# Performance work log

Hardware: AMD Instinct MI355X
Metric: run time of the kernel (lower is better)

Reference implementation:

```python
import jax, jax.numpy as jnp
import numpy as np

T, B, E, H = 2048, 2, 1024, 16
DH = E // H
SCALE = DH ** -0.5
NEG = jnp.finfo(jnp.float32).min


def setup_inputs() -> dict:
    key = jax.random.key(0)
    ks = jax.random.split(key, 10)
    s = 0.02
    query = jax.random.normal(ks[0], (T, B, E), dtype=jnp.float32)
    key_padding_mask = jax.random.randint(ks[1], (B, T), 0, 2).astype(bool)
    # causal additive mask, broadcastable over (bsz, heads, tgt, src)
    causal = jnp.triu(jnp.ones((T, T), dtype=bool), k=1)
    attn_mask = jnp.where(causal, NEG, 0.0).astype(jnp.float32)[None, None]
    Wq = jax.random.normal(ks[2], (E, E), jnp.float32) * s
    bq = jax.random.normal(ks[3], (E,), jnp.float32) * s
    Wk = jax.random.normal(ks[4], (E, E), jnp.float32) * s
    bk = jax.random.normal(ks[5], (E,), jnp.float32) * s
    Wv = jax.random.normal(ks[6], (E, E), jnp.float32) * s
    bv = jax.random.normal(ks[7], (E,), jnp.float32) * s
    Wo = jax.random.normal(ks[8], (E, E), jnp.float32) * s
    bo = jax.random.normal(ks[9], (E,), jnp.float32) * s
    return {"query": query, "key_padding_mask": key_padding_mask, "attn_mask": attn_mask,
            "Wq": Wq, "bq": bq, "Wk": Wk, "bk": bk, "Wv": Wv, "bv": bv, "Wo": Wo, "bo": bo}


def _heads(x):
    # [T, B, E] -> [B, H, T, DH]
    return x.reshape(T, B, H, DH).transpose(1, 2, 0, 3)


def reference(query, key_padding_mask, attn_mask, Wq, bq, Wk, bk, Wv, bv, Wo, bo):
    # projections (torch Linear: x @ W.T + b); q scaled as in module
    q = _heads((query @ Wq.T + bq) * SCALE)          # [B,H,T,DH]
    k = _heads(query @ Wk.T + bk)                    # [B,H,S,DH] (self-attn: S=T)
    v = _heads(query @ Wv.T + bv)
    scores = jnp.einsum('bhtd,bhsd->bhts', q, k)     # [B,H,T,S]
    scores = scores + attn_mask                      # additive causal mask
    # key_padding_mask True -> masked_fill with dtype min
    scores = jnp.where(key_padding_mask[:, None, None, :], NEG, scores)
    probs = jax.nn.softmax(scores, axis=-1)
    ctx = jnp.einsum('bhts,bhsd->bhtd', probs, v)    # [B,H,T,DH]
    ctx = ctx.transpose(2, 0, 1, 3).reshape(T, B, E) # back to [T,B,E]
    return ctx @ Wo.T + bo
```

## Files before the change

kernel.cpp:

```cpp
#include <hip/hip_runtime.h>
#include <hip/hip_bf16.h>
#include <stdint.h>

typedef unsigned short u16;
typedef uint32_t u32;
typedef unsigned long long u64;
typedef __attribute__((ext_vector_type(8))) short bf16x8;
typedef __attribute__((ext_vector_type(4))) float f32x4;
typedef __attribute__((ext_vector_type(16))) float f32x16;
typedef __attribute__((ext_vector_type(4))) u32 u32x4;

#define T_SEQ 2048

__device__ __forceinline__ float bf2f(u16 u) {
  union { u32 i; float f; } v; v.i = ((u32)u) << 16; return v.f;
}
__device__ __forceinline__ u16 f2bf(float f) {
  union { float f; u32 i; } v; v.f = f;
  u32 u = v.i;
  return (u16)((u + 0x7fffu + ((u >> 16) & 1u)) >> 16);
}

#if __has_builtin(__builtin_amdgcn_exp2f)
#define EXP2F(x) __builtin_amdgcn_exp2f(x)
#else
#define EXP2F(x) exp2f(x)
#endif

__device__ __forceinline__ u32 permpack(float lo, float hi) {
#if __has_builtin(__builtin_amdgcn_perm)
  return __builtin_amdgcn_perm(__float_as_uint(hi), __float_as_uint(lo), 0x07060302u);
#else
  return (__float_as_uint(hi) & 0xFFFF0000u) | (__float_as_uint(lo) >> 16);
#endif
}

__device__ __forceinline__ void gload_lds16(const void* g, void* l) {
  __builtin_amdgcn_global_load_lds(
      (const __attribute__((address_space(1))) void*)g,
      (__attribute__((address_space(3))) void*)l, 16, 0, 0);
}

__global__ __launch_bounds__(256) void cvt_kernel(const float* __restrict__ src,
                                                  u16* __restrict__ dst, int n) {
  int i = (blockIdx.x * 256 + threadIdx.x) * 4;
  if (i + 3 < n) {
    const float4 v = *(const float4*)(src + i);
    ushort4 o;
    o.x = f2bf(v.x); o.y = f2bf(v.y); o.z = f2bf(v.z); o.w = f2bf(v.w);
    *(ushort4*)(dst + i) = o;
  }
}

__global__ __launch_bounds__(256) void cvt4_kernel(
    const float* __restrict__ s0, const float* __restrict__ s1,
    const float* __restrict__ s2, const float* __restrict__ s3,
    u16* __restrict__ dst) {
  const int z = blockIdx.y;
  const float* src = (z == 0) ? s0 : (z == 1) ? s1 : (z == 2) ? s2 : s3;
  int i = (blockIdx.x * 256 + threadIdx.x) * 4;
  const float4 v = *(const float4*)(src + i);
  ushort4 o;
  o.x = f2bf(v.x); o.y = f2bf(v.y); o.z = f2bf(v.z); o.w = f2bf(v.w);
  *(ushort4*)(dst + (size_t)z * 1048576 + i) = o;
}

__device__ __forceinline__ void gemm_core_128x128(
    f32x4 acc[2][4], const u16* __restrict__ A, const u16* __restrict__ Bw,
    int bm, int bn, u16* As, u16* Bs)
{
  const int tid = threadIdx.x;
  const int w = tid >> 6, lane = tid & 63, g = lane >> 4, c = lane & 15;
  const int wr = (w & 3) * 32, wc = (w >> 2) * 64;
  for (int k0 = 0; k0 < 1024; k0 += 64) {
    __syncthreads();
    #pragma unroll
    for (int is = 0; is < 2; ++is) {
      int o = (is*8 + w)*1024 + lane*16;
      int row = o >> 7, c16 = (o >> 4) & 7;
      gload_lds16(A + (size_t)(bm*128 + row)*1024 + k0 + (c16 ^ (row & 7))*8,
                  (char*)As + (is*8 + w)*1024);
    }
    #pragma unroll
    for (int is = 0; is < 2; ++is) {
      int o = (is*8 + w)*1024 + lane*16;
      int row = o >> 7, c16 = (o >> 4) & 7;
      gload_lds16(Bw + (size_t)(bn*128 + row)*1024 + k0 + (c16 ^ (row & 7))*8,
                  (char*)Bs + (is*8 + w)*1024);
    }
    __syncthreads();
    bf16x8 af[2][2], bfr[4][2];
    #pragma unroll
    for (int mf = 0; mf < 2; ++mf)
      #pragma unroll
      for (int kc = 0; kc < 2; ++kc) {
        int row = wr + mf*16 + c;
        int colb = kc*64 + g*16;
        af[mf][kc] = *(const bf16x8*)((const char*)As + row*128 + (colb ^ ((row & 7) << 4)));
      }
    #pragma unroll
    for (int nf = 0; nf < 4; ++nf)
      #pragma unroll
      for (int kc = 0; kc < 2; ++kc) {
        int row = wc + nf*16 + c;
        int colb = kc*64 + g*16;
        bfr[nf][kc] = *(const bf16x8*)((const char*)Bs + row*128 + (colb ^ ((row & 7) << 4)));
      }
    #pragma unroll
    for (int mf = 0; mf < 2; ++mf)
      #pragma unroll
      for (int nf = 0; nf < 4; ++nf)
        #pragma unroll
        for (int kc = 0; kc < 2; ++kc)
          acc[mf][nf] = __builtin_amdgcn_mfma_f32_16x16x32_bf16(
              af[mf][kc], bfr[nf][kc], acc[mf][nf], 0, 0, 0);
  }
}

__global__ __launch_bounds__(512, 2) void gemm_qkv(
    const u16* __restrict__ Abf, const u16* __restrict__ Wbf,
    const float* __restrict__ bq, const float* __restrict__ bk,
    const float* __restrict__ bv, u16* __restrict__ qkvh)
{
  __shared__ __align__(16) u16 As[128*64];
  __shared__ __align__(16) u16 Bs[128*64];
  f32x4 acc[2][4];
  #pragma unroll
  for (int mf = 0; mf < 2; ++mf)
    #pragma unroll
    for (int nf = 0; nf < 4; ++nf) acc[mf][nf] = (f32x4){0.f,0.f,0.f,0.f};
  const int bx = blockIdx.x;
  const int bm = (bx & 7) * 4 + (bx >> 3);
  gemm_core_128x128(acc, Abf, Wbf, bm, blockIdx.y, As, Bs);
  const int tid = threadIdx.x, w = tid >> 6, lane = tid & 63, g = lane >> 4, c = lane & 15;
  const int wr = (w & 3) * 32, wc = (w >> 2) * 64;
  #pragma unroll
  for (int mf = 0; mf < 2; ++mf)
    #pragma unroll
    for (int nf = 0; nf < 4; ++nf) {
      int col = blockIdx.y*128 + wc + nf*16 + c;
      int z = col >> 10, colz = col & 1023;
      const float* bias = (z == 0) ? bq : (z == 1) ? bk : bv;
      float bcol = bias[colz];
      float scl = (z == 0) ? 0.18033688011112043f : 1.0f;
      int h = colz >> 6, d = colz & 63;
      u16* dst = qkvh + (size_t)z * 4194304;
      #pragma unroll
      for (int r = 0; r < 4; ++r) {
        int row = bm*128 + wr + mf*16 + g*4 + r;
        int t = row >> 1, bb = row & 1;
        float v = (acc[mf][nf][r] + bcol) * scl;
        dst[(size_t)(bb*16 + h)*131072 + (size_t)t*64 + d] = f2bf(v);
      }
    }
}

__global__ __launch_bounds__(512, 2) void gemm_out(
    const u16* __restrict__ ctx2, const u16* __restrict__ Wobf,
    const float* __restrict__ bo, float* __restrict__ out)
{
  __shared__ __align__(16) u16 As[128*64];
  __shared__ __align__(16) u16 Bs[128*64];
  f32x4 acc[2][4];
  #pragma unroll
  for (int mf = 0; mf < 2; ++mf)
    #pragma unroll
    for (int nf = 0; nf < 4; ++nf) acc[mf][nf] = (f32x4){0.f,0.f,0.f,0.f};
  const int bx = blockIdx.x;
  const int bm = (bx & 7) * 4 + (bx >> 3);
  gemm_core_128x128(acc, ctx2, Wobf, bm, blockIdx.y, As, Bs);
  const int tid = threadIdx.x, w = tid >> 6, lane = tid & 63, g = lane >> 4, c = lane & 15;
  const int wr = (w & 3) * 32, wc = (w >> 2) * 64;
  #pragma unroll
  for (int mf = 0; mf < 2; ++mf)
    #pragma unroll
    for (int nf = 0; nf < 4; ++nf) {
      int col = blockIdx.y*128 + wc + nf*16 + c;
      float bcol = bo[col];
      #pragma unroll
      for (int r = 0; r < 4; ++r) {
        int row = bm*128 + wr + mf*16 + g*4 + r;
        out[(size_t)row*1024 + col] = acc[mf][nf][r] + bcol;
      }
    }
}

__global__ __launch_bounds__(256) void vtrans_kernel(const u16* __restrict__ Vh,
                                                     u16* __restrict__ Vt,
                                                     float* __restrict__ vs) {
  __shared__ u16 tile[64][72];
  const int bh = blockIdx.x >> 5, tc = blockIdx.x & 31;
  const int t0 = tc * 64;
  const int tid = threadIdx.x;
  {
    const int tl = tid >> 2, d0 = (tid & 3) * 16;
    const u16* src = Vh + (size_t)bh*131072 + (size_t)(t0 + tl)*64 + d0;
    bf16x8 a = *(const bf16x8*)src;
    bf16x8 b2 = *(const bf16x8*)(src + 8);
    #pragma unroll
    for (int j = 0; j < 8; ++j) {
      tile[d0 + j][tl] = (u16)a[j];
      tile[d0 + 8 + j][tl] = (u16)b2[j];
    }
  }
  __syncthreads();
  {
    const int d = tid >> 2, tq = (tid & 3) * 16;
    bf16x8 o0, o1;
    float s = 0.f;
    #pragma unroll
    for (int j = 0; j < 8; ++j) {
      u16 x0 = tile[d][tq + j], x1 = tile[d][tq + 8 + j];
      o0[j] = (short)x0; o1[j] = (short)x1;
      s += bf2f(x0) + bf2f(x1);
    }
    u16* dst = Vt + (size_t)bh*131072 + (size_t)d*2048 + t0 + tq;
    *(bf16x8*)dst = o0;
    *(bf16x8*)(dst + 8) = o1;
    s += __shfl_xor(s, 1, 64);
    s += __shfl_xor(s, 2, 64);
    if ((tid & 3) == 0) atomicAdd(&vs[bh*64 + d], s);
  }
}

#define ZERO16 (f32x16){0.f,0.f,0.f,0.f,0.f,0.f,0.f,0.f,0.f,0.f,0.f,0.f,0.f,0.f,0.f,0.f}
#define NEGINF (-__builtin_inff())

__global__ __launch_bounds__(256, 2) void flash_attn(
    const u16* __restrict__ Qh, const u16* __restrict__ Kh,
    const u16* __restrict__ Vt, const int* __restrict__ kpm,
    const float* __restrict__ vsum, u16* __restrict__ ctx2,
    u16* __restrict__ pctx, float* __restrict__ pml)
{
  __shared__ __align__(16) u16 Kl[2][4096];
  __shared__ __align__(16) u16 Vl[2][4096];

  const int tid = threadIdx.x;
  const int w = tid >> 6, lane = tid & 63;
  const int l31 = lane & 31, hi = lane >> 5;

  const int id = blockIdx.x;
  const int xcd = id & 7, rest = id >> 3;
  const int bh = xcd * 4 + (rest & 3);
  const int pr = rest >> 2;
  const u64 k0t = 0x9AA5BBCC6DDEE7FFULL, k1t = 0x94883210ULL;
  const u64 m0t = 0x0102101021010210ULL, m1t = 0x12102222ULL;
  const int k  = (int)(((pr < 16) ? (k0t >> (pr*4)) : (k1t >> ((pr-16)*4))) & 15);
  const int md = (int)(((pr < 16) ? (m0t >> (pr*4)) : (m1t >> ((pr-16)*4))) & 3);
  const int NS = (md == 2) ? 1 : 2, ch = md & 1;

  const int ntmax = 2*k + 2;
  const int b = bh >> 4, h = bh & 15;
  const size_t hbase = (size_t)bh * 131072;
  int lo, hicap;
  if (NS == 1) { lo = 0; hicap = ntmax; }
  else { lo = ch ? (k+1) : 0; hicap = ch ? ntmax : (k+1); }
  const int q = 128*k + 32*w + l31;
  const int myNt = 2*k + 1 + (w >> 1);

  bf16x8 qfrag[4];
  #pragma unroll
  for (int kt = 0; kt < 4; ++kt)
    qfrag[kt] = *(const bf16x8*)(Qh + hbase + (size_t)q*64 + kt*16 + hi*8);

  {
    const int s0t = lo * 64;
    const int jb = (w & 1) * 4;
    if (w < 2) {
      #pragma unroll
      for (int is = 0; is < 4; ++is) {
        int o = (jb + is)*1024 + lane*16;
        int row = o >> 7, c16 = (o >> 4) & 7;
        gload_lds16(Kh + hbase + (size_t)(s0t + row)*64 + (c16 ^ (row & 7))*8,
                    (char*)Kl[0] + (jb + is)*1024);
      }
    } else {
      #pragma unroll
      for (int is = 0; is < 4; ++is) {
        int o = (jb + is)*1024 + lane*16;
        int row = o >> 7, c16 = (o >> 4) & 7;
        gload_lds16(Vt + hbase + (size_t)row*2048 + s0t + (c16 ^ (row & 7))*8,
                    (char*)Vl[0] + (jb + is)*1024);
      }
    }
  }
  int kpmv_cur = kpm[b*T_SEQ + lo*64 + lane];
  int kpmv_nxt = 0;
  __syncthreads();

  float mrow = NEGINF, lrow = 0.f;
  f32x16 cacc0 = ZERO16, cacc1 = ZERO16;

  for (int t = lo; t < hicap; ++t) {
    const int cur = (t - lo) & 1, nxt = cur ^ 1;
    const int s0 = t * 64;
    const bool notLast = (t + 1 < hicap);
    const bool diag = (t >= myNt - 1);

    if (notLast) {
      const int s0n = s0 + 64;
      const int jb = (w & 1) * 4;
      if (w < 2) {
        #pragma unroll
        for (int is = 0; is < 4; ++is) {
          int o = (jb + is)*1024 + lane*16;
          int row = o >> 7, c16 = (o >> 4) & 7;
          gload_lds16(Kh + hbase + (size_t)(s0n + row)*64 + (c16 ^ (row & 7))*8,
                      (char*)Kl[nxt] + (jb + is)*1024);
        }
      } else {
        #pragma unroll
        for (int is = 0; is < 4; ++is) {
          int o = (jb + is)*1024 + lane*16;
          int row = o >> 7, c16 = (o >> 4) & 7;
          gload_lds16(Vt + hbase + (size_t)row*2048 + s0n + (c16 ^ (row & 7))*8,
                      (char*)Vl[nxt] + (jb + is)*1024);
        }
      }
      kpmv_nxt = kpm[b*T_SEQ + s0n + lane];
    }

    bf16x8 kreg[2][4], vf[2][4];
    #pragma unroll
    for (int sub = 0; sub < 2; ++sub)
      #pragma unroll
      for (int kt = 0; kt < 4; ++kt) {
        int row = sub*32 + l31;
        int colb = kt*32 + hi*16;
        kreg[sub][kt] = *(const bf16x8*)((const char*)Kl[cur] + row*128 + (colb ^ ((row & 7) << 4)));
        vf[sub][kt]   = *(const bf16x8*)((const char*)Vl[cur] + row*128 + (colb ^ ((row & 7) << 4)));
      }

    f32x16 st0 = ZERO16, st1 = ZERO16;
    __builtin_amdgcn_s_setprio(1);
    #pragma unroll
    for (int kt = 0; kt < 4; ++kt) {
      st0 = __builtin_amdgcn_mfma_f32_32x32x16_bf16(kreg[0][kt], qfrag[kt], st0, 0, 0, 0);
      st1 = __builtin_amdgcn_mfma_f32_32x32x16_bf16(kreg[1][kt], qfrag[kt], st1, 0, 0, 0);
    }
    __builtin_amdgcn_s_setprio(0);

    {
      const u64 mask = __ballot(kpmv_cur != 0);
      const u32 m0 = (u32)mask, m1 = (u32)(mask >> 32);
      const u64 m4 = mask >> 4;
      const u32 m4l = (u32)m4, m4h = (u32)(m4 >> 32);
      const u32 w0 = hi ? m4l : m0;
      const u32 w1 = hi ? m4h : m1;
      const int lim = q - s0 - 4*hi;
      #pragma unroll
      for (int m = 0; m < 4; ++m) {
        u32 nib0 = (w0 >> (m*8)) & 15u;
        u32 nib1 = (w1 >> (m*8)) & 15u;
        if (diag) {
          int t0c = lim - m*8;       int c0 = min(max(t0c + 1, 0), 4);
          int t1c = lim - 32 - m*8;  int c1 = min(max(t1c + 1, 0), 4);
          nib0 |= (0xFu << c0) & 0xFu;
          nib1 |= (0xFu << c1) & 0xFu;
        }
        #pragma unroll
        for (int r = 0; r < 4; ++r) {
          if ((nib0 >> r) & 1) st0[m*4 + r] = NEGINF;
          if ((nib1 >> r) & 1) st1[m*4 + r] = NEGINF;
        }
      }
      float t8[8];
      #pragma unroll
      for (int i = 0; i < 8; ++i)
        t8[i] = fmaxf(fmaxf(st0[i], st0[i+8]), fmaxf(st1[i], st1[i+8]));
      float t4a = fmaxf(t8[0], t8[4]), t4b = fmaxf(t8[1], t8[5]);
      float t4c = fmaxf(t8[2], t8[6]), t4d = fmaxf(t8[3], t8[7]);
      float rm = fmaxf(fmaxf(t4a, t4b), fmaxf(t4c, t4d));
      rm = fmaxf(rm, __shfl_xor(rm, 32, 64));

      const bool need = (rm > mrow + 8.f) || (mrow < -1e30f);
      if (__any(need)) {
        const float mn = fmaxf(mrow, rm);
        const float sc = (mn < -1e30f) ? 1.f : EXP2F(mrow - mn);
        mrow = mn;
        lrow *= sc;
        #pragma unroll
        for (int i = 0; i < 16; ++i) { cacc0[i] *= sc; cacc1[i] *= sc; }
      }
      const bool dead = (mrow < -1e30f);
      float a0 = 0.f, a1 = 0.f, a2 = 0.f, a3 = 0.f;
      #pragma unroll
      for (int i = 0; i < 16; i += 4) {
        float p0 = dead ? 0.f : EXP2F(st0[i+0] - mrow); st0[i+0] = p0; a0 += p0;
        float p1 = dead ? 0.f : EXP2F(st0[i+1] - mrow); st0[i+1] = p1; a1 += p1;
        float p2 = dead ? 0.f : EXP2F(st0[i+2] - mrow); st0[i+2] = p2; a2 += p2;
        float p3 = dead ? 0.f : EXP2F(st0[i+3] - mrow); st0[i+3] = p3; a3 += p3;
      }
      #pragma unroll
      for (int i = 0; i < 16; i += 4) {
        float p0 = dead ? 0.f : EXP2F(st1[i+0] - mrow); st1[i+0] = p0; a0 += p0;
        float p1 = dead ? 0.f : EXP2F(st1[i+1] - mrow); st1[i+1] = p1; a1 += p1;
        float p2 = dead ? 0.f : EXP2F(st1[i+2] - mrow); st1[i+2] = p2; a2 += p2;
        float p3 = dead ? 0.f : EXP2F(st1[i+3] - mrow); st1[i+3] = p3; a3 += p3;
      }
      float ps = (a0 + a1) + (a2 + a3);
      ps += __shfl_xor(ps, 32, 64);
      lrow += ps;
    }

    u32 pk[8][2];
    #pragma unroll
    for (int m = 0; m < 4; ++m) {
      pk[m][0]   = permpack(st0[m*4+0], st0[m*4+1]);
      pk[m][1]   = permpack(st0[m*4+2], st0[m*4+3]);
      pk[4+m][0] = permpack(st1[m*4+0], st1[m*4+1]);
      pk[4+m][1] = permpack(st1[m*4+2], st1[m*4+3]);
    }
    bf16x8 pf[4];
    #pragma unroll
    for (int ks = 0; ks < 4; ++ks) {
      u32 own0 = pk[2*ks][0],   own1 = pk[2*ks][1];
      u32 oth0 = pk[2*ks+1][0], oth1 = pk[2*ks+1][1];
      u32 r0 = __shfl_xor(hi ? own0 : oth0, 32, 64);
      u32 r1 = __shfl_xor(hi ? own1 : oth1, 32, 64);
      u32 w0 = hi ? r0 : own0;
      u32 w1 = hi ? r1 : own1;
      u32 w2 = hi ? oth0 : r0;
      u32 w3 = hi ? oth1 : r1;
      u32x4 wv = {w0, w1, w2, w3};
      pf[ks] = __builtin_bit_cast(bf16x8, wv);
    }

    __builtin_amdgcn_s_setprio(1);
    #pragma unroll
    for (int ks = 0; ks < 4; ++ks)
      cacc0 = __builtin_amdgcn_mfma_f32_32x32x16_bf16(vf[0][ks], pf[ks], cacc0, 0, 0, 0);
    #pragma unroll
    for (int ks = 0; ks < 4; ++ks)
      cacc1 = __builtin_amdgcn_mfma_f32_32x32x16_bf16(vf[1][ks], pf[ks], cacc1, 0, 0, 0);
    __builtin_amdgcn_s_setprio(0);

    kpmv_cur = kpmv_nxt;
    if (notLast) __syncthreads();
  }

  if (NS == 1) {
    const bool dead = (lrow == 0.f);
    const float rl = dead ? 0.f : 1.f / lrow;
    #pragma unroll
    for (int subd = 0; subd < 2; ++subd) {
      #pragma unroll
      for (int m = 0; m < 4; ++m) {
        const int d0 = subd*32 + hi*4 + m*8;
        float v0 = (subd ? cacc1[m*4+0] : cacc0[m*4+0]) * rl;
        float v1 = (subd ? cacc1[m*4+1] : cacc0[m*4+1]) * rl;
        float v2 = (subd ? cacc1[m*4+2] : cacc0[m*4+2]) * rl;
        float v3 = (subd ? cacc1[m*4+3] : cacc0[m*4+3]) * rl;
        if (dead) {
          const float* vs = vsum + bh*64 + d0;
          v0 = vs[0] * (1.0f/2048.0f);
          v1 = vs[1] * (1.0f/2048.0f);
          v2 = vs[2] * (1.0f/2048.0f);
          v3 = vs[3] * (1.0f/2048.0f);
        }
        ushort4 o;
        o.x = f2bf(v0); o.y = f2bf(v1); o.z = f2bf(v2); o.w = f2bf(v3);
        *(ushort4*)(ctx2 + (size_t)(q*2 + b)*1024 + h*64 + d0) = o;
      }
    }
  } else {
    const int slot = ((bh << 3) + (k - 8))*2 + ch;
    const int row = w*32 + l31;
    u16* pc = pctx + ((size_t)slot*128 + row)*64;
    #pragma unroll
    for (int subd = 0; subd < 2; ++subd) {
      #pragma unroll
      for (int m = 0; m < 4; ++m) {
        const int d0 = subd*32 + hi*4 + m*8;
        const f32x16& cc = subd ? cacc1 : cacc0;
        ushort4 o;
        o.x = f2bf(cc[m*4+0]); o.y = f2bf(cc[m*4+1]);
        o.z = f2bf(cc[m*4+2]); o.w = f2bf(cc[m*4+3]);
        *(ushort4*)(pc + d0) = o;
      }
    }
    if (!hi) {
      float2 ml; ml.x = mrow; ml.y = lrow;
      *(float2*)(pml + ((size_t)slot*128 + row)*2) = ml;
    }
  }
}

__global__ __launch_bounds__(64) void combine_kernel(
    const u16* __restrict__ pctx, const float* __restrict__ pml,
    const float* __restrict__ vsum, u16* __restrict__ ctx2)
{
  const int qtm = blockIdx.x, bh = blockIdx.y;
  const int qt = 32 + qtm;
  const int k = qt >> 2, wq = qt & 3;
  const int b = bh >> 4, h = bh & 15;
  const int lane = threadIdx.x;
  const int qr = lane >> 1, d0 = (lane & 1) * 32;
  const int slot0 = ((bh << 3) + (k - 8))*2;
  const int row = wq*32 + qr;
  const float* ml0 = pml + ((size_t)slot0*128 + row)*2;
  const float* ml1 = pml + ((size_t)(slot0+1)*128 + row)*2;
  const float m1 = ml0[0], l1 = ml0[1];
  const float m2 = ml1[0], l2 = ml1[1];
  const float ms = fmaxf(m1, m2);
  bool dead = (ms == NEGINF);
  const float w1 = dead ? 0.f : EXP2F(m1 - ms);
  const float w2 = dead ? 0.f : EXP2F(m2 - ms);
  const float lt = w1*l1 + w2*l2;
  dead = dead || (lt == 0.f);
  const float rl = dead ? 0.f : 1.f / lt;
  const u16* c1 = pctx + ((size_t)slot0*128 + row)*64 + d0;
  const u16* c2 = pctx + ((size_t)(slot0+1)*128 + row)*64 + d0;
  const int qrow = qt*32 + qr;
  u16* dst = ctx2 + (size_t)(qrow*2 + b)*1024 + h*64 + d0;
  #pragma unroll
  for (int g2 = 0; g2 < 4; ++g2) {
    bf16x8 a = *(const bf16x8*)(c1 + g2*8);
    bf16x8 bb = *(const bf16x8*)(c2 + g2*8);
    bf16x8 o;
    #pragma unroll
    for (int j = 0; j < 8; ++j) {
      float v = (w1*bf2f((u16)a[j]) + w2*bf2f((u16)bb[j])) * rl;
      if (dead) v = vsum[bh*64 + d0 + g2*8 + j] * (1.0f/2048.0f);
      o[j] = (short)f2bf(v);
    }
    *(bf16x8*)(dst + g2*8) = o;
  }
}

extern "C" void kernel_launch(void* const* d_in, const int* in_sizes, int n_in,
                              void* d_out, int out_size, void* d_ws, size_t ws_size,
                              hipStream_t stream) {
  const float* query = (const float*)d_in[0];
  const int*   kpm   = (const int*)d_in[1];
  const float* Wq = (const float*)d_in[3];
  const float* bq = (const float*)d_in[4];
  const float* Wk = (const float*)d_in[5];
  const float* bk = (const float*)d_in[6];
  const float* Wv = (const float*)d_in[7];
  const float* bv = (const float*)d_in[8];
  const float* Wo = (const float*)d_in[9];
  const float* bo = (const float*)d_in[10];

  char* ws = (char*)d_ws;
  u16*   qbf  = (u16*)(ws);
  u16*   Vt   = (u16*)(ws);
  u16*   wbf  = (u16*)(ws + 8388608);
  u16*   qkvh = (u16*)(ws + 16777216);
  u16*   pctx = (u16*)(ws + 33554432);
  u16*   ctx2 = (u16*)(ws + 41943040);
  float* vsum = (float*)(ws + 50331648);
  float* pml  = (float*)(ws + 50339840);

  cvt_kernel<<<dim3(4096), 256, 0, stream>>>(query, qbf, 4194304);
  cvt4_kernel<<<dim3(1024, 4), 256, 0, stream>>>(Wq, Wk, Wv, Wo, wbf);

  hipMemsetAsync(vsum, 0, 2048 * sizeof(float), stream);

  gemm_qkv<<<dim3(32, 24), 512, 0, stream>>>(qbf, wbf, bq, bk, bv, qkvh);
  vtrans_kernel<<<dim3(1024), 256, 0, stream>>>(qkvh + 2*4194304, Vt, vsum);
  flash_attn<<<dim3(768), 256, 0, stream>>>(qkvh, qkvh + 1*4194304,
                                            Vt, kpm, vsum, ctx2, pctx, pml);
  combine_kernel<<<dim3(32, 32), 64, 0, stream>>>(pctx, pml, vsum, ctx2);
  gemm_out<<<dim3(32, 8), 512, 0, stream>>>(ctx2, wbf + 3*1048576, bo, (float*)d_out);
}
```

Baseline: 134.4 us.

## Double-buffer GEMM LDS tiles, premask scores via accumulator init, use permlane32 swaps

```diff
diff --git a/kernel.cpp b/kernel.cpp
--- a/kernel.cpp
+++ b/kernel.cpp
@@ -8,6 +8,7 @@
 typedef __attribute__((ext_vector_type(8))) short bf16x8;
 typedef __attribute__((ext_vector_type(4))) float f32x4;
 typedef __attribute__((ext_vector_type(16))) float f32x16;
+typedef __attribute__((ext_vector_type(2))) unsigned int u32x2;
 typedef __attribute__((ext_vector_type(4))) u32 u32x4;
 
 #define T_SEQ 2048
@@ -33,6 +34,24 @@
 #else
   return (__float_as_uint(hi) & 0xFFFF0000u) | (__float_as_uint(lo) >> 16);
 #endif
+}
+
+__device__ __forceinline__ void plswap(u32& a, u32& b) {
+#if __has_builtin(__builtin_amdgcn_permlane32_swap)
+  u32x2 r = __builtin_amdgcn_permlane32_swap(a, b, false, false);
+  a = r[0]; b = r[1];
+#else
+  u32 ra = __shfl_xor(a, 32, 64), rb = __shfl_xor(b, 32, 64);
+  const bool hi_ = (threadIdx.x & 32) != 0;
+  u32 na = hi_ ? rb : a;
+  u32 nb = hi_ ? b : ra;
+  a = na; b = nb;
+#endif
+}
+__device__ __forceinline__ float othhalf(float x, bool ishi) {
+  u32 a = __float_as_uint(x), b = a;
+  plswap(a, b);
+  return __uint_as_float(ishi ? a : b);
 }
 
 __device__ __forceinline__ void gload_lds16(const void* g, void* l) {
@@ -72,23 +91,33 @@
   const int tid = threadIdx.x;
   const int w = tid >> 6, lane = tid & 63, g = lane >> 4, c = lane & 15;
   const int wr = (w & 3) * 32, wc = (w >> 2) * 64;
-  for (int k0 = 0; k0 < 1024; k0 += 64) {
-    __syncthreads();
+
+  auto stage = [&](int buf, int k0) {
     #pragma unroll
     for (int is = 0; is < 2; ++is) {
       int o = (is*8 + w)*1024 + lane*16;
       int row = o >> 7, c16 = (o >> 4) & 7;
       gload_lds16(A + (size_t)(bm*128 + row)*1024 + k0 + (c16 ^ (row & 7))*8,
-                  (char*)As + (is*8 + w)*1024);
+                  (char*)As + buf*16384 + (is*8 + w)*1024);
     }
     #pragma unroll
     for (int is = 0; is < 2; ++is) {
       int o = (is*8 + w)*1024 + lane*16;
       int row = o >> 7, c16 = (o >> 4) & 7;
       gload_lds16(Bw + (size_t)(bn*128 + row)*1024 + k0 + (c16 ^ (row & 7))*8,
-                  (char*)Bs + (is*8 + w)*1024);
-    }
-    __syncthreads();
+                  (char*)Bs + buf*16384 + (is*8 + w)*1024);
+    }
+  };
+
+  stage(0, 0);
+  asm volatile("s_waitcnt vmcnt(0)" ::: "memory");
+  __syncthreads();
+
+  for (int k0 = 0; k0 < 1024; k0 += 64) {
+    const int cur = (k0 >> 6) & 1, nxt = cur ^ 1;
+    const bool more = (k0 + 64 < 1024);
+    if (more) stage(nxt, k0 + 64);
+
     bf16x8 af[2][2], bfr[4][2];
     #pragma unroll
     for (int mf = 0; mf < 2; ++mf)
@@ -96,7 +125,7 @@
       for (int kc = 0; kc < 2; ++kc) {
         int row = wr + mf*16 + c;
         int colb = kc*64 + g*16;
-        af[mf][kc] = *(const bf16x8*)((const char*)As + row*128 + (colb ^ ((row & 7) << 4)));
+        af[mf][kc] = *(const bf16x8*)((const char*)As + cur*16384 + row*128 + (colb ^ ((row & 7) << 4)));
       }
     #pragma unroll
     for (int nf = 0; nf < 4; ++nf)
@@ -104,7 +133,7 @@
       for (int kc = 0; kc < 2; ++kc) {
         int row = wc + nf*16 + c;
         int colb = kc*64 + g*16;
-        bfr[nf][kc] = *(const bf16x8*)((const char*)Bs + row*128 + (colb ^ ((row & 7) << 4)));
+        bfr[nf][kc] = *(const bf16x8*)((const char*)Bs + cur*16384 + row*128 + (colb ^ ((row & 7) << 4)));
       }
     #pragma unroll
     for (int mf = 0; mf < 2; ++mf)
@@ -114,6 +143,11 @@
         for (int kc = 0; kc < 2; ++kc)
           acc[mf][nf] = __builtin_amdgcn_mfma_f32_16x16x32_bf16(
               af[mf][kc], bfr[nf][kc], acc[mf][nf], 0, 0, 0);
+
+    if (more) {
+      asm volatile("s_waitcnt vmcnt(0)" ::: "memory");
+      __syncthreads();
+    }
   }
 }
 
@@ -122,8 +156,8 @@
     const float* __restrict__ bq, const float* __restrict__ bk,
     const float* __restrict__ bv, u16* __restrict__ qkvh)
 {
-  __shared__ __align__(16) u16 As[128*64];
-  __shared__ __align__(16) u16 Bs[128*64];
+  __shared__ __align__(16) u16 As[2][128*64];
+  __shared__ __align__(16) u16 Bs[2][128*64];
   f32x4 acc[2][4];
   #pragma unroll
   for (int mf = 0; mf < 2; ++mf)
@@ -131,7 +165,7 @@
     for (int nf = 0; nf < 4; ++nf) acc[mf][nf] = (f32x4){0.f,0.f,0.f,0.f};
   const int bx = blockIdx.x;
   const int bm = (bx & 7) * 4 + (bx >> 3);
-  gemm_core_128x128(acc, Abf, Wbf, bm, blockIdx.y, As, Bs);
+  gemm_core_128x128(acc, Abf, Wbf, bm, blockIdx.y, &As[0][0], &Bs[0][0]);
   const int tid = threadIdx.x, w = tid >> 6, lane = tid & 63, g = lane >> 4, c = lane & 15;
   const int wr = (w & 3) * 32, wc = (w >> 2) * 64;
   #pragma unroll
@@ -159,8 +193,8 @@
     const u16* __restrict__ ctx2, const u16* __restrict__ Wobf,
     const float* __restrict__ bo, float* __restrict__ out)
 {
-  __shared__ __align__(16) u16 As[128*64];
-  __shared__ __align__(16) u16 Bs[128*64];
+  __shared__ __align__(16) u16 As[2][128*64];
+  __shared__ __align__(16) u16 Bs[2][128*64];
   f32x4 acc[2][4];
   #pragma unroll
   for (int mf = 0; mf < 2; ++mf)
@@ -168,7 +202,7 @@
     for (int nf = 0; nf < 4; ++nf) acc[mf][nf] = (f32x4){0.f,0.f,0.f,0.f};
   const int bx = blockIdx.x;
   const int bm = (bx & 7) * 4 + (bx >> 3);
-  gemm_core_128x128(acc, ctx2, Wobf, bm, blockIdx.y, As, Bs);
+  gemm_core_128x128(acc, ctx2, Wobf, bm, blockIdx.y, &As[0][0], &Bs[0][0]);
   const int tid = threadIdx.x, w = tid >> 6, lane = tid & 63, g = lane >> 4, c = lane & 15;
   const int wr = (w & 3) * 32, wc = (w >> 2) * 64;
   #pragma unroll
@@ -320,50 +354,56 @@
       kpmv_nxt = kpm[b*T_SEQ + s0n + lane];
     }
 
-    bf16x8 kreg[2][4], vf[2][4];
-    #pragma unroll
-    for (int sub = 0; sub < 2; ++sub)
-      #pragma unroll
-      for (int kt = 0; kt < 4; ++kt) {
-        int row = sub*32 + l31;
-        int colb = kt*32 + hi*16;
-        kreg[sub][kt] = *(const bf16x8*)((const char*)Kl[cur] + row*128 + (colb ^ ((row & 7) << 4)));
-        vf[sub][kt]   = *(const bf16x8*)((const char*)Vl[cur] + row*128 + (colb ^ ((row & 7) << 4)));
-      }
-
-    f32x16 st0 = ZERO16, st1 = ZERO16;
-    __builtin_amdgcn_s_setprio(1);
-    #pragma unroll
-    for (int kt = 0; kt < 4; ++kt) {
-      st0 = __builtin_amdgcn_mfma_f32_32x32x16_bf16(kreg[0][kt], qfrag[kt], st0, 0, 0, 0);
-      st1 = __builtin_amdgcn_mfma_f32_32x32x16_bf16(kreg[1][kt], qfrag[kt], st1, 0, 0, 0);
-    }
-    __builtin_amdgcn_s_setprio(0);
-
+    u32 kill0 = 0, kill1 = 0;
     {
       const u64 mask = __ballot(kpmv_cur != 0);
       const u32 m0 = (u32)mask, m1 = (u32)(mask >> 32);
       const u64 m4 = mask >> 4;
       const u32 m4l = (u32)m4, m4h = (u32)(m4 >> 32);
-      const u32 w0 = hi ? m4l : m0;
-      const u32 w1 = hi ? m4h : m1;
+      const u32 w0m = hi ? m4l : m0;
+      const u32 w1m = hi ? m4h : m1;
       const int lim = q - s0 - 4*hi;
       #pragma unroll
       for (int m = 0; m < 4; ++m) {
-        u32 nib0 = (w0 >> (m*8)) & 15u;
-        u32 nib1 = (w1 >> (m*8)) & 15u;
+        u32 nib0 = (w0m >> (m*8)) & 15u;
+        u32 nib1 = (w1m >> (m*8)) & 15u;
         if (diag) {
           int t0c = lim - m*8;       int c0 = min(max(t0c + 1, 0), 4);
           int t1c = lim - 32 - m*8;  int c1 = min(max(t1c + 1, 0), 4);
           nib0 |= (0xFu << c0) & 0xFu;
           nib1 |= (0xFu << c1) & 0xFu;
         }
-        #pragma unroll
-        for (int r = 0; r < 4; ++r) {
-          if ((nib0 >> r) & 1) st0[m*4 + r] = NEGINF;
-          if ((nib1 >> r) & 1) st1[m*4 + r] = NEGINF;
-        }
-      }
+        kill0 |= nib0 << (m*4);
+        kill1 |= nib1 << (m*4);
+      }
+    }
+    f32x16 st0, st1;
+    #pragma unroll
+    for (int i = 0; i < 16; ++i) {
+      st0[i] = ((kill0 >> i) & 1u) ? NEGINF : 0.f;
+      st1[i] = ((kill1 >> i) & 1u) ? NEGINF : 0.f;
+    }
+
+    bf16x8 kreg[2][4], vf[2][4];
+    #pragma unroll
+    for (int sub = 0; sub < 2; ++sub)
+      #pragma unroll
+      for (int kt = 0; kt < 4; ++kt) {
+        int row = sub*32 + l31;
+        int colb = kt*32 + hi*16;
+        kreg[sub][kt] = *(const bf16x8*)((const char*)Kl[cur] + row*128 + (colb ^ ((row & 7) << 4)));
+        vf[sub][kt]   = *(const bf16x8*)((const char*)Vl[cur] + row*128 + (colb ^ ((row & 7) << 4)));
+      }
+
+    __builtin_amdgcn_s_setprio(1);
+    #pragma unroll
+    for (int kt = 0; kt < 4; ++kt) {
+      st0 = __builtin_amdgcn_mfma_f32_32x32x16_bf16(kreg[0][kt], qfrag[kt], st0, 0, 0, 0);
+      st1 = __builtin_amdgcn_mfma_f32_32x32x16_bf16(kreg[1][kt], qfrag[kt], st1, 0, 0, 0);
+    }
+    __builtin_amdgcn_s_setprio(0);
+
+    {
       float t8[8];
       #pragma unroll
       for (int i = 0; i < 8; ++i)
@@ -371,7 +411,7 @@
       float t4a = fmaxf(t8[0], t8[4]), t4b = fmaxf(t8[1], t8[5]);
       float t4c = fmaxf(t8[2], t8[6]), t4d = fmaxf(t8[3], t8[7]);
       float rm = fmaxf(fmaxf(t4a, t4b), fmaxf(t4c, t4d));
-      rm = fmaxf(rm, __shfl_xor(rm, 32, 64));
+      rm = fmaxf(rm, othhalf(rm, hi != 0));
 
       const bool need = (rm > mrow + 8.f) || (mrow < -1e30f);
       if (__any(need)) {
@@ -399,7 +439,7 @@
         float p3 = dead ? 0.f : EXP2F(st1[i+3] - mrow); st1[i+3] = p3; a3 += p3;
       }
       float ps = (a0 + a1) + (a2 + a3);
-      ps += __shfl_xor(ps, 32, 64);
+      ps += othhalf(ps, hi != 0);
       lrow += ps;
     }
 
@@ -414,15 +454,11 @@
     bf16x8 pf[4];
     #pragma unroll
     for (int ks = 0; ks < 4; ++ks) {
-      u32 own0 = pk[2*ks][0],   own1 = pk[2*ks][1];
-      u32 oth0 = pk[2*ks+1][0], oth1 = pk[2*ks+1][1];
-      u32 r0 = __shfl_xor(hi ? own0 : oth0, 32, 64);
-      u32 r1 = __shfl_xor(hi ? own1 : oth1, 32, 64);
-      u32 w0 = hi ? r0 : own0;
-      u32 w1 = hi ? r1 : own1;
-      u32 w2 = hi ? oth0 : r0;
-      u32 w3 = hi ? oth1 : r1;
-      u32x4 wv = {w0, w1, w2, w3};
+      u32 w0p = pk[2*ks][0], w2p = pk[2*ks+1][0];
+      u32 w1p = pk[2*ks][1], w3p = pk[2*ks+1][1];
+      plswap(w0p, w2p);
+      plswap(w1p, w3p);
+      u32x4 wv = {w0p, w1p, w2p, w3p};
       pf[ks] = __builtin_bit_cast(bf16x8, wv);
     }
 
```

Result: slower. 137.4 us (+2.3%).
